# Kernel tuning notes

Measured on AMD Instinct MI355X. Metric: run time of the kernel, lower is better.

The kernel has to match this reference:

```python
import jax, jax.numpy as jnp
import numpy as np

VOCAB = 32000
WORDVEC = 256
HIDDEN = 512
NULL_TOKEN = 0


def setup_inputs() -> dict:
    key = jax.random.key(0)
    ks = jax.random.split(key, 8)
    N, Tp1 = 16, 257
    captions = jax.random.randint(ks[0], (N, Tp1), 0, VOCAB, dtype=jnp.int64 if jax.config.jax_enable_x64 else jnp.int32)
    W_embed = jax.random.normal(ks[1], (VOCAB, WORDVEC), jnp.float32) / 100.0
    Wx = jax.random.normal(ks[2], (WORDVEC, 4 * HIDDEN), jnp.float32) / np.sqrt(WORDVEC).astype(np.float32)
    Wh = jax.random.normal(ks[3], (HIDDEN, 4 * HIDDEN), jnp.float32) / np.sqrt(HIDDEN).astype(np.float32)
    b = jnp.zeros((4 * HIDDEN,), jnp.float32)
    W_vocab = jax.random.normal(ks[4], (HIDDEN, VOCAB), jnp.float32) / np.sqrt(HIDDEN).astype(np.float32)
    b_vocab = jnp.zeros((VOCAB,), jnp.float32)
    h_init = jax.random.normal(ks[5], (HIDDEN,), jnp.float32)
    return {"captions": captions, "W_embed": W_embed, "Wx": Wx, "Wh": Wh,
            "b": b, "W_vocab": W_vocab, "b_vocab": b_vocab, "h_init": h_init}


def reference(captions, W_embed, Wx, Wh, b, W_vocab, b_vocab, h_init):
    cap_in = captions[:, :-1]   # [N, T]
    cap_out = captions[:, 1:]   # [N, T]
    mask = (cap_out != NULL_TOKEN).astype(jnp.float32)
    N = cap_in.shape[0]
    H = h_init.shape[0]

    # Embedding lookup: [N, T, D]
    x = W_embed[cap_in]
    # Precompute input projections as one big GEMM: [T, N, 4H]
    xw = jnp.einsum('ntd,dk->tnk', x, Wx) + b

    h0 = jnp.tile(h_init, (N, 1))          # [N, H]
    c0 = jnp.zeros_like(h0)                 # lstm_forward starts c at zeros

    def step(carry, a_x):
        h, c = carry
        a = a_x + h @ Wh                    # [N, 4H]
        i, f, o, g = jnp.split(a, 4, axis=-1)
        i = jax.nn.sigmoid(i)
        f = jax.nn.sigmoid(f)
        o = jax.nn.sigmoid(o)
        g = jnp.tanh(g)
        c = f * c + i * g
        h = o * jnp.tanh(c)
        return (h, c), h

    _, hs = jax.lax.scan(step, (h0, c0), xw)  # hs: [T, N, H]

    # Temporal affine: [N, T, V]
    logits = jnp.einsum('tnh,hv->ntv', hs, W_vocab) + b_vocab
    logp = jax.nn.log_softmax(logits, axis=-1)
    nll = -jnp.take_along_axis(logp, cap_out[..., None], axis=-1)[..., 0]
    loss = jnp.sum(nll * mask) / N
    return loss
```

## Files before the change

kernel.cpp:

```cpp
#include <hip/hip_runtime.h>

#define VOCAB   32000
#define WORDVEC 256
#define HIDDEN  512
#define TSTEPS  256
#define NBATCH  16
#define NROWS   (TSTEPS*NBATCH)
#define GATES   (4*HIDDEN)
#define NVB     125
#define NWG     32
#define NVBLK   8000
#define SPINCAP (1<<16)

typedef __attribute__((ext_vector_type(8))) short short8;
typedef __attribute__((ext_vector_type(4))) float f32x4;
typedef unsigned long long u64;

#define AGLOAD(p) __hip_atomic_load((p), __ATOMIC_RELAXED, __HIP_MEMORY_SCOPE_AGENT)
#define MFMA16(a,b,c) __builtin_amdgcn_mfma_f32_16x16x32_bf16((a),(b),(c),0,0,0)

__device__ __forceinline__ unsigned short f2bf(float x){
    union { float f; unsigned int u; } v; v.f = x;
    unsigned int r = v.u + 0x7fffu + ((v.u >> 16) & 1u);
    return (unsigned short)(r >> 16);
}

__global__ __launch_bounds__(256) void prep_all(const int* __restrict__ captions,
        const float* __restrict__ Wemb, const float* __restrict__ Wx,
        const float* __restrict__ b, float* __restrict__ xw,
        const float* __restrict__ Wh, unsigned short* __restrict__ Whp,
        const float* __restrict__ h_init, u64* __restrict__ hx,
        const float* __restrict__ Wv, unsigned short* __restrict__ WvP,
        int* __restrict__ prog){
    __shared__ float s[64][65];
    float (*xs)[WORDVEC] = (float(*)[WORDVEC])s;
    __shared__ int toks[8];
    int bid = blockIdx.x;
    int tid = threadIdx.x;
    if (bid < 512){
        int r0 = bid * 8;
        if (tid < 8){
            int r = r0 + tid; int t = r >> 4, n = r & 15;
            toks[tid] = captions[n*257 + t];
        }
        __syncthreads();
        for (int i = 0; i < 8; ++i){
            int lin = tid + i*256;
            int ri = lin >> 8, d = lin & 255;
            xs[ri][d] = Wemb[(long)toks[ri]*WORDVEC + d];
        }
        __syncthreads();
        float4 b0 = *(const float4*)(b + tid*4);
        float4 b1 = *(const float4*)(b + 1024 + tid*4);
        float acc[8][8];
        for (int ri = 0; ri < 8; ++ri){
            acc[ri][0]=b0.x; acc[ri][1]=b0.y; acc[ri][2]=b0.z; acc[ri][3]=b0.w;
            acc[ri][4]=b1.x; acc[ri][5]=b1.y; acc[ri][6]=b1.z; acc[ri][7]=b1.w;
        }
        for (int d = 0; d < WORDVEC; ++d){
            float4 w0 = *(const float4*)(Wx + (long)d*GATES + tid*4);
            float4 w1 = *(const float4*)(Wx + (long)d*GATES + 1024 + tid*4);
            #pragma unroll
            for (int ri = 0; ri < 8; ++ri){
                float xv = xs[ri][d];
                acc[ri][0] += xv*w0.x; acc[ri][1] += xv*w0.y;
                acc[ri][2] += xv*w0.z; acc[ri][3] += xv*w0.w;
                acc[ri][4] += xv*w1.x; acc[ri][5] += xv*w1.y;
                acc[ri][6] += xv*w1.z; acc[ri][7] += xv*w1.w;
            }
        }
        for (int ri = 0; ri < 8; ++ri){
            float4 o0 = {acc[ri][0],acc[ri][1],acc[ri][2],acc[ri][3]};
            float4 o1 = {acc[ri][4],acc[ri][5],acc[ri][6],acc[ri][7]};
            *(float4*)(xw + (long)(r0+ri)*GATES + tid*4) = o0;
            *(float4*)(xw + (long)(r0+ri)*GATES + 1024 + tid*4) = o1;
        }
    } else if (bid < 544){
        int w = bid - 512;
        for (int item = tid; item < 4096; item += 256){
            int f = item >> 6;
            int L = item & 63;
            int kt = f >> 2, nt = f & 3;
            int q = L >> 4, ln = L & 15;
            int col = nt*HIDDEN + w*16 + ln;
            short8 vvec;
            for (int jj = 0; jj < 8; ++jj){
                int k = kt*32 + q*8 + jj;
                vvec[jj] = (short)f2bf(Wh[(long)k*GATES + col]);
            }
            *(short8*)(Whp + ((long)w*4096 + item)*8) = vvec;
        }
    } else if (bid < 560){
        if (bid == 544 && tid < 32) prog[tid] = 0;
        int p = (bid - 544)*256 + tid;
        int fq = p >> 6;
        int j  = (p & 3) * 2;
        int u0 = (fq>>2)*32 + (fq&3)*8 + j;
        u64 pk = (u64)f2bf(h_init[u0]) | ((u64)f2bf(h_init[u0+1]) << 16);
        hx[p] = pk;
    } else {
        int tile = bid - 560;
        int v0 = (tile >> 3) * 64;
        int k0 = (tile & 7) * 64;
        for (int i = 0; i < 16; ++i){
            int lin = tid + i*256;
            int kk = lin >> 6, vv = lin & 63;
            s[kk][vv] = Wv[(long)(k0+kk)*VOCAB + v0 + vv];
        }
        __syncthreads();
        for (int i = 0; i < 2; ++i){
            int lr = tid + i*256;
            int f  = lr >> 6;
            int vbl = f >> 1, ktl = f & 1;
            int L = lr & 63, q = L >> 4, ln = L & 15;
            short8 o;
            #pragma unroll
            for (int j = 0; j < 8; ++j)
                o[j] = (short)f2bf(s[ktl*32 + q*8 + j][vbl*16 + ln]);
            long vb = (long)(tile >> 3)*4 + vbl;
            long kt = (long)(tile & 7)*2 + ktl;
            *(short8*)(WvP + ((vb*16 + kt)*64 + L)*8) = o;
        }
    }
}

__global__ __launch_bounds__(256) void lstm_vocab(const float* __restrict__ xw,
        const unsigned short* __restrict__ Whp, u64* __restrict__ hx,
        unsigned short* __restrict__ hsP, int* __restrict__ prog,
        const unsigned short* __restrict__ WvP, const float* __restrict__ bvoc,
        const int* __restrict__ captions, float* __restrict__ pmax,
        float* __restrict__ psum, float* __restrict__ tlog){
    __shared__ unsigned int hstage[4096];
    __shared__ float a_s[4][16][16];
    __shared__ int   tgt_s[64];
    __shared__ float wmax_s[4][64], wsum_s[4][64];
    int tid = threadIdx.x;

    if (blockIdx.x >= NWG){
        int vid = blockIdx.x - NWG;
        int pri = vid / 2000;
        int idx = vid % 2000;
        int p   = (idx & 7)*250 + (idx >> 3);
        int bn  = p >> 4;
        int bm  = (p & 15)*4 + pri;
        int need = (pri + 1) * 4;

        if (tid == 0){
            int cnt = 0;
            for (;;){
                int mn = 1 << 30;
                for (int i = 0; i < 32; ++i){
                    int pv = AGLOAD(&prog[i]);
                    mn = pv < mn ? pv : mn;
                }
                if (mn >= need) break;
                __builtin_amdgcn_s_sleep(32);
                if (++cnt > SPINCAP) break;
            }
        }
        __syncthreads();

        int wv = tid >> 6, L = tid & 63;
        int q = L >> 4, ln = L & 15;
        if (tid < 64){
            int rg = bm*64 + tid;
            tgt_s[tid] = captions[(rg >> 8)*257 + (rg & 255) + 1];
        }
        __syncthreads();
        f32x4 acc[4][4];
        for (int mt=0;mt<4;++mt) for (int nt=0;nt<4;++nt) acc[mt][nt] = (f32x4){0.f,0.f,0.f,0.f};
        int colb = bn*256 + wv*64;
        const unsigned short* aB = hsP + ((long)(bm*4)*16)*512 + (long)L*8;
        const unsigned short* bB = WvP + ((long)(bn*16 + wv*4)*16)*512 + (long)L*8;
        #pragma unroll 1
        for (int kt = 0; kt < 16; ++kt){
            const short8* aK = (const short8*)(aB + (long)kt*512);
            const short8* bK = (const short8*)(bB + (long)kt*512);
            short8 a0 = aK[0],    a1 = aK[1024];
            short8 b0 = bK[0],    b1 = bK[1024];
            acc[0][0] = MFMA16(a0,b0,acc[0][0]); acc[0][1] = MFMA16(a0,b1,acc[0][1]);
            acc[1][0] = MFMA16(a1,b0,acc[1][0]); acc[1][1] = MFMA16(a1,b1,acc[1][1]);
            __builtin_amdgcn_sched_barrier(0);
            short8 b2 = bK[2048], b3 = bK[3072];
            acc[0][2] = MFMA16(a0,b2,acc[0][2]); acc[0][3] = MFMA16(a0,b3,acc[0][3]);
            acc[1][2] = MFMA16(a1,b2,acc[1][2]); acc[1][3] = MFMA16(a1,b3,acc[1][3]);
            __builtin_amdgcn_sched_barrier(0);
            short8 a2 = aK[2048], a3 = aK[3072];
            acc[2][2] = MFMA16(a2,b2,acc[2][2]); acc[2][3] = MFMA16(a2,b3,acc[2][3]);
            acc[3][2] = MFMA16(a3,b2,acc[3][2]); acc[3][3] = MFMA16(a3,b3,acc[3][3]);
            __builtin_amdgcn_sched_barrier(0);
            u64 bKo = (u64)bK; asm volatile("" : "+v"(bKo));
            const short8* bK2 = (const short8*)bKo;
            short8 c0 = bK2[0], c1 = bK2[1024];
            acc[2][0] = MFMA16(a2,c0,acc[2][0]); acc[2][1] = MFMA16(a2,c1,acc[2][1]);
            acc[3][0] = MFMA16(a3,c0,acc[3][0]); acc[3][1] = MFMA16(a3,c1,acc[3][1]);
            __builtin_amdgcn_sched_barrier(0);
        }
        float bv[4];
        #pragma unroll
        for (int nt=0;nt<4;++nt) bv[nt] = bvoc[colb + nt*16 + ln];
        #pragma unroll
        for (int mt=0;mt<4;++mt) for (int nt=0;nt<4;++nt) for (int r=0;r<4;++r)
            acc[mt][nt][r] += bv[nt];
        #pragma unroll
        for (int mt=0;mt<4;++mt)
            #pragma unroll
            for (int nt=0;nt<4;++nt)
                #pragma unroll
                for (int r=0;r<4;++r){
                    int rl = mt*16 + q*4 + r;
                    int tg = tgt_s[rl] - colb;
                    if (tg == nt*16 + ln) tlog[bm*64 + rl] = acc[mt][nt][r];
                }
        #pragma unroll
        for (int mt=0;mt<4;++mt){
            #pragma unroll
            for (int r=0;r<4;++r){
                float m = fmaxf(fmaxf(acc[mt][0][r],acc[mt][1][r]), fmaxf(acc[mt][2][r],acc[mt][3][r]));
                for (int d=1; d<16; d<<=1) m = fmaxf(m, __shfl_xor(m, d, 16));
                float s = __expf(acc[mt][0][r]-m) + __expf(acc[mt][1][r]-m)
                        + __expf(acc[mt][2][r]-m) + __expf(acc[mt][3][r]-m);
                for (int d=1; d<16; d<<=1) s += __shfl_xor(s, d, 16);
                if (ln == 0){ int rl = mt*16 + q*4 + r; wmax_s[wv][rl] = m; wsum_s[wv][rl] = s; }
            }
        }
        __syncthreads();
        if (tid < 64){
            float M = fmaxf(fmaxf(wmax_s[0][tid],wmax_s[1][tid]), fmaxf(wmax_s[2][tid],wmax_s[3][tid]));
            float S = 0.f;
            for (int ww=0; ww<4; ++ww) S += wsum_s[ww][tid]*__expf(wmax_s[ww][tid]-M);
            pmax[(long)bn*NROWS + bm*64 + tid] = M;
            psum[(long)bn*NROWS + bm*64 + tid] = S;
        }
        return;
    }

    int w = blockIdx.x;
    int wv = tid >> 6;
    int L = tid & 63;
    int q = L >> 4, ln = L & 15;
    int s_idx = tid >> 4, jl = tid & 15;

    short8 bw[16];
    #pragma unroll
    for (int kt = 0; kt < 16; ++kt)
        bw[kt] = *(const short8*)(Whp + ((long)w*4096 + (kt*4+wv)*64 + L)*8);

    float c_r = 0.f;
    int fq_pub = (w>>1)*4 + (w&1)*2 + (jl>>3);
    int pubIdx = fq_pub*64 + s_idx*4 + ((jl>>1)&3);
    int kt_h = w >> 1;
    int q_h  = ((w & 1) << 1) | (jl >> 3);
    int j_h  = jl & 7;
    unsigned int* hsP32 = (unsigned int*)hsP;

    for (int t = 0; t < TSTEPS; ++t){
        long xb = (long)(t*16 + s_idx)*GATES + w*16 + jl;
        float xg0 = xw[xb], xg1 = xw[xb+512], xg2 = xw[xb+1024], xg3 = xw[xb+1536];

        const u64* hr = hx + (t & 1)*4096;
        u64*       hw = hx + ((t+1) & 1)*4096;

        u64 v[16];
        #pragma unroll
        for (int i = 0; i < 16; ++i)
            v[i] = AGLOAD(hr + tid + i*256);
        for (;;){
            u64 bad = 0;
            #pragma unroll
            for (int i = 0; i < 16; ++i) bad |= (v[i] >> 32) ^ (u64)(unsigned)t;
            if (!bad) break;
            #pragma unroll
            for (int i = 0; i < 16; ++i)
                v[i] = AGLOAD(hr + tid + i*256);
        }
        #pragma unroll
        for (int i = 0; i < 16; ++i) hstage[tid + i*256] = (unsigned)v[i];
        __syncthreads();

        f32x4 acc = {0.f,0.f,0.f,0.f};
        #pragma unroll
        for (int kt = 0; kt < 16; ++kt){
            short8 a = *(const short8*)((const unsigned short*)hstage + (kt*256 + q*64 + ln*4)*2);
            acc = MFMA16(a, bw[kt], acc);
        }
        #pragma unroll
        for (int r = 0; r < 4; ++r) a_s[wv][q*4 + r][ln] = acc[r];
        __syncthreads();

        float ai = a_s[0][s_idx][jl] + xg0;
        float af = a_s[1][s_idx][jl] + xg1;
        float ao = a_s[2][s_idx][jl] + xg2;
        float ag = a_s[3][s_idx][jl] + xg3;
        float ig = 1.f/(1.f + __expf(-ai));
        float fg = 1.f/(1.f + __expf(-af));
        float og = 1.f/(1.f + __expf(-ao));
        float gg = 2.f/(1.f + __expf(-2.f*ag)) - 1.f;
        c_r = fg*c_r + ig*gg;
        float hv = og * (2.f/(1.f + __expf(-2.f*c_r)) - 1.f);
        unsigned short hb = f2bf(hv);

        int hv32 = (int)hb;
        int other = __shfl(hv32, L ^ 1);
        int rb = s_idx*16 + (t >> 4);
        if ((jl & 1) == 0){
            u64 pk = (u64)(unsigned short)hv32
                   | ((u64)(unsigned short)other << 16)
                   | ((u64)(unsigned)(t+1) << 32);
            __hip_atomic_store(hw + pubIdx, pk, __ATOMIC_RELAXED, __HIP_MEMORY_SCOPE_AGENT);
            unsigned int hp = (unsigned int)(unsigned short)hv32
                            | ((unsigned int)(unsigned short)other << 16);
            __hip_atomic_store(hsP32 + (((long)(rb*16 + kt_h))*64 + q_h*16 + (t & 15))*4 + (j_h >> 1),
                               hp, __ATOMIC_RELAXED, __HIP_MEMORY_SCOPE_AGENT);
        }
        if ((t & 15) == 15){
            asm volatile("s_waitcnt vmcnt(0)" ::: "memory");
            __syncthreads();
            if (tid == 0)
                __hip_atomic_store(&prog[w], (t >> 4) + 1, __ATOMIC_RELAXED, __HIP_MEMORY_SCOPE_AGENT);
        }
    }
}

__global__ __launch_bounds__(256) void reduce_loss(const float* __restrict__ pmax,
        const float* __restrict__ psum, const float* __restrict__ tlog,
        const int* __restrict__ captions, float* __restrict__ out){
    int r = blockIdx.x*256 + threadIdx.x;
    float M = -1e30f;
    #pragma unroll 5
    for (int p=0;p<NVB;++p) M = fmaxf(M, pmax[(long)p*NROWS + r]);
    float S = 0.f;
    #pragma unroll 5
    for (int p=0;p<NVB;++p) S += psum[(long)p*NROWS + r]*__expf(pmax[(long)p*NROWS + r]-M);
    float lse = M + logf(S);
    float nll = lse - tlog[r];
    int tok = captions[(r >> 8)*257 + (r & 255) + 1];
    float val = (tok != 0) ? nll : 0.f;
    __shared__ float red[256];
    red[threadIdx.x] = val; __syncthreads();
    for (int s=128; s>0; s>>=1){
        if (threadIdx.x < s) red[threadIdx.x] += red[threadIdx.x+s];
        __syncthreads();
    }
    if (threadIdx.x == 0) atomicAdd(out, red[0] * (1.0f/16.0f));
}

extern "C" void kernel_launch(void* const* d_in, const int* in_sizes, int n_in,
                              void* d_out, int out_size, void* d_ws, size_t ws_size,
                              hipStream_t stream){
    const int*   captions = (const int*)  d_in[0];
    const float* Wemb     = (const float*)d_in[1];
    const float* Wx       = (const float*)d_in[2];
    const float* Wh       = (const float*)d_in[3];
    const float* b        = (const float*)d_in[4];
    const float* Wv       = (const float*)d_in[5];
    const float* bvoc     = (const float*)d_in[6];
    const float* h_init   = (const float*)d_in[7];

    char* ws = (char*)d_ws;
    float*          xw   = (float*)         (ws + 0);
    unsigned short* WvP  = (unsigned short*)(ws + 33554432);
    unsigned short* hsP  = (unsigned short*)(ws + 66322432);
    float*          pmax = (float*)         (ws + 70516736);
    float*          psum = (float*)         (ws + 72564736);
    float*          tlog = (float*)         (ws + 74612736);
    unsigned short* Whp  = (unsigned short*)(ws + 74629120);
    u64*            hx   = (u64*)           (ws + 76726272);
    int*            prog = (int*)           (ws + 76791808);

    float* out_f = (float*)d_out;

    (void)hipMemsetAsync(d_out, 0, sizeof(float), stream);

    hipLaunchKernelGGL(prep_all,    dim3(4560),       dim3(256), 0, stream,
                       captions, Wemb, Wx, b, xw, Wh, Whp, h_init, hx, Wv, WvP, prog);
    hipLaunchKernelGGL(lstm_vocab,  dim3(NWG+NVBLK),  dim3(256), 0, stream,
                       xw, Whp, hx, hsP, prog, WvP, bvoc, captions, pmax, psum, tlog);
    hipLaunchKernelGGL(reduce_loss, dim3(16),         dim3(256), 0, stream,
                       pmax, psum, tlog, captions, out_f);
}
```

Baseline: 1.006 ms.

## Reorder hidden-state rows time-major and sync vocab tiles on per-chunk counters

Stores LSTM outputs time-major, so each 64-row vocab tile covers 4 timesteps for all 16 sequences and can start as soon as one 16-step chunk finishes, rather than after a strided progress requirement. Replaces the per-workgroup progress array scan with an atomic counter per chunk, so consumers poll one word instead of 32. Adds a cheap wavefront-wide spin on a small hint subset of the hidden-state buffer before the full load. The vocab tiles are launched in a simple bm-major order, which changes scheduling and the overlap between the recurrence and the vocab GEMM.

Result: slower. 1.068 ms (+6.2%).

```diff
diff --git a/kernel.cpp b/kernel.cpp
--- a/kernel.cpp
+++ b/kernel.cpp
@@ -31,7 +31,7 @@
         const float* __restrict__ Wh, unsigned short* __restrict__ Whp,
         const float* __restrict__ h_init, u64* __restrict__ hx,
         const float* __restrict__ Wv, unsigned short* __restrict__ WvP,
-        int* __restrict__ prog){
+        int* __restrict__ chunkcnt){
     __shared__ float s[64][65];
     float (*xs)[WORDVEC] = (float(*)[WORDVEC])s;
     __shared__ int toks[8];
@@ -91,7 +91,7 @@
             *(short8*)(Whp + ((long)w*4096 + item)*8) = vvec;
         }
     } else if (bid < 560){
-        if (bid == 544 && tid < 32) prog[tid] = 0;
+        if (bid == 544 && tid < 16) chunkcnt[tid] = 0;
         int p = (bid - 544)*256 + tid;
         int fq = p >> 6;
         int j  = (p & 3) * 2;
@@ -126,7 +126,7 @@
 
 __global__ __launch_bounds__(256) void lstm_vocab(const float* __restrict__ xw,
         const unsigned short* __restrict__ Whp, u64* __restrict__ hx,
-        unsigned short* __restrict__ hsP, int* __restrict__ prog,
+        unsigned short* __restrict__ hsP, int* __restrict__ chunkcnt,
         const unsigned short* __restrict__ WvP, const float* __restrict__ bvoc,
         const int* __restrict__ captions, float* __restrict__ pmax,
         float* __restrict__ psum, float* __restrict__ tlog){
@@ -138,23 +138,14 @@
 
     if (blockIdx.x >= NWG){
         int vid = blockIdx.x - NWG;
-        int pri = vid / 2000;
-        int idx = vid % 2000;
-        int p   = (idx & 7)*250 + (idx >> 3);
-        int bn  = p >> 4;
-        int bm  = (p & 15)*4 + pri;
-        int need = (pri + 1) * 4;
+        int bm  = vid / 125;
+        int bn  = vid % 125;
+        int needc = bm >> 2;
 
         if (tid == 0){
             int cnt = 0;
-            for (;;){
-                int mn = 1 << 30;
-                for (int i = 0; i < 32; ++i){
-                    int pv = AGLOAD(&prog[i]);
-                    mn = pv < mn ? pv : mn;
-                }
-                if (mn >= need) break;
-                __builtin_amdgcn_s_sleep(32);
+            while (AGLOAD(&chunkcnt[needc]) < NWG){
+                __builtin_amdgcn_s_sleep(8);
                 if (++cnt > SPINCAP) break;
             }
         }
@@ -164,7 +155,7 @@
         int q = L >> 4, ln = L & 15;
         if (tid < 64){
             int rg = bm*64 + tid;
-            tgt_s[tid] = captions[(rg >> 8)*257 + (rg & 255) + 1];
+            tgt_s[tid] = captions[(rg & 15)*257 + (rg >> 4) + 1];
         }
         __syncthreads();
         f32x4 acc[4][4];
@@ -253,6 +244,8 @@
     int q_h  = ((w & 1) << 1) | (jl >> 3);
     int j_h  = jl & 7;
     unsigned int* hsP32 = (unsigned int*)hsP;
+    int ww_ = tid & 31;
+    int hintIdx = ((ww_>>1)*4 + (ww_&1)*2)*64;
 
     for (int t = 0; t < TSTEPS; ++t){
         long xb = (long)(t*16 + s_idx)*GATES + w*16 + jl;
@@ -261,6 +254,13 @@
         const u64* hr = hx + (t & 1)*4096;
         u64*       hw = hx + ((t+1) & 1)*4096;
 
+        {
+            const u64* hintp = hr + hintIdx;
+            for (;;){
+                u64 hv_ = AGLOAD(hintp);
+                if (__all((unsigned)(hv_ >> 32) == (unsigned)t)) break;
+            }
+        }
         u64 v[16];
         #pragma unroll
         for (int i = 0; i < 16; ++i)
@@ -302,7 +302,6 @@
 
         int hv32 = (int)hb;
         int other = __shfl(hv32, L ^ 1);
-        int rb = s_idx*16 + (t >> 4);
         if ((jl & 1) == 0){
             u64 pk = (u64)(unsigned short)hv32
                    | ((u64)(unsigned short)other << 16)
@@ -310,14 +309,13 @@
             __hip_atomic_store(hw + pubIdx, pk, __ATOMIC_RELAXED, __HIP_MEMORY_SCOPE_AGENT);
             unsigned int hp = (unsigned int)(unsigned short)hv32
                             | ((unsigned int)(unsigned short)other << 16);
-            __hip_atomic_store(hsP32 + (((long)(rb*16 + kt_h))*64 + q_h*16 + (t & 15))*4 + (j_h >> 1),
+            __hip_atomic_store(hsP32 + (((long)(t*16 + kt_h))*64 + q_h*16 + s_idx)*4 + (j_h >> 1),
                                hp, __ATOMIC_RELAXED, __HIP_MEMORY_SCOPE_AGENT);
         }
         if ((t & 15) == 15){
             asm volatile("s_waitcnt vmcnt(0)" ::: "memory");
             __syncthreads();
-            if (tid == 0)
-                __hip_atomic_store(&prog[w], (t >> 4) + 1, __ATOMIC_RELAXED, __HIP_MEMORY_SCOPE_AGENT);
+            if (tid == 0) atomicAdd(&chunkcnt[t >> 4], 1);
         }
     }
 }
@@ -334,7 +332,7 @@
     for (int p=0;p<NVB;++p) S += psum[(long)p*NROWS + r]*__expf(pmax[(long)p*NROWS + r]-M);
     float lse = M + logf(S);
     float nll = lse - tlog[r];
-    int tok = captions[(r >> 8)*257 + (r & 255) + 1];
+    int tok = captions[(r & 15)*257 + (r >> 4) + 1];
     float val = (tok != 0) ? nll : 0.f;
     __shared__ float red[256];
     red[threadIdx.x] = val; __syncthreads();
@@ -366,16 +364,16 @@
     float*          tlog = (float*)         (ws + 74612736);
     unsigned short* Whp  = (unsigned short*)(ws + 74629120);
     u64*            hx   = (u64*)           (ws + 76726272);
-    int*            prog = (int*)           (ws + 76791808);
+    int*            cct  = (int*)           (ws + 76791808);
 
     float* out_f = (float*)d_out;
 
     (void)hipMemsetAsync(d_out, 0, sizeof(float), stream);
 
     hipLaunchKernelGGL(prep_all,    dim3(4560),       dim3(256), 0, stream,
-                       captions, Wemb, Wx, b, xw, Wh, Whp, h_init, hx, Wv, WvP, prog);
+                       captions, Wemb, Wx, b, xw, Wh, Whp, h_init, hx, Wv, WvP, cct);
     hipLaunchKernelGGL(lstm_vocab,  dim3(NWG+NVBLK),  dim3(256), 0, stream,
-                       xw, Whp, hx, hsP, prog, WvP, bvoc, captions, pmax, psum, tlog);
+                       xw, Whp, hx, hsP, cct, WvP, bvoc, captions, pmax, psum, tlog);
     hipLaunchKernelGGL(reduce_loss, dim3(16),         dim3(256), 0, stream,
                        pmax, psum, tlog, captions, out_f);
 }
```
